# Optimization experiments

Measured on AMD Instinct MI355X. Metric: run time of the kernel, lower is better.

The kernel has to match this reference:

```python
import jax, jax.numpy as jnp
import numpy as np

DIM, HEADS, RANK = 768, 12, 64
HEAD_DIM = DIM // HEADS

def _xavier(key, shape):
    fan_in, fan_out = shape[1], shape[0]
    std = (2.0 / (fan_in + fan_out)) ** 0.5
    return std * jax.random.normal(key, shape, dtype=jnp.float32)

def setup_inputs() -> dict:
    key = jax.random.key(0)
    ks = jax.random.split(key, 12)
    B, N = 8, 1024
    x = jax.random.normal(ks[0], (B, N, DIM), dtype=jnp.float32)
    params = {}
    for i, nm in enumerate(['Q', 'K', 'V']):
        params[f'W_{nm}0'] = _xavier(ks[1 + 3 * i], (DIM, RANK))
        params[f'W_{nm}1'] = _xavier(ks[2 + 3 * i], (HEADS, RANK))
        params[f'W_{nm}2'] = _xavier(ks[3 + 3 * i], (HEAD_DIM, RANK))
    proj_w = _xavier(ks[10], (DIM, DIM))
    proj_b = jnp.zeros((DIM,), dtype=jnp.float32)
    return dict(x=x, W_Q0=params['W_Q0'], W_Q1=params['W_Q1'], W_Q2=params['W_Q2'],
                W_K0=params['W_K0'], W_K1=params['W_K1'], W_K2=params['W_K2'],
                W_V0=params['W_V0'], W_V1=params['W_V1'], W_V2=params['W_V2'],
                proj_w=proj_w, proj_b=proj_b)

def _cp_proj(xh, W2, W1, W0, B, N, H, hd):
    # xh: [B,N,H,hd]; contract head_dim with W2 and heads with W1 -> [B,N,R], then expand to dim via W0
    t = jnp.einsum('blnd,dr,nr->blr', xh, W2, W1)
    out = jnp.einsum('blr,mr->blm', t, W0)          # [B,N,dim]
    return out.reshape(B, N, H, hd).transpose(0, 2, 1, 3)  # [B,H,N,hd]

def reference(x, W_Q0, W_Q1, W_Q2, W_K0, W_K1, W_K2, W_V0, W_V1, W_V2, proj_w, proj_b):
    B, N, C = x.shape
    H = W_Q1.shape[0]
    hd = C // H
    scale = hd ** -0.5
    xh = x.reshape(B, N, H, hd)
    q = _cp_proj(xh, W_Q2, W_Q1, W_Q0, B, N, H, hd)
    k = _cp_proj(xh, W_K2, W_K1, W_K0, B, N, H, hd)
    v = _cp_proj(xh, W_V2, W_V1, W_V0, B, N, H, hd)
    attn = jax.nn.softmax(jnp.einsum('bhqd,bhkd->bhqk', q, k) * scale, axis=-1)
    out = jnp.einsum('bhqk,bhkd->bhqd', attn, v).transpose(0, 2, 1, 3).reshape(B, N, C)
    return out @ proj_w.T + proj_b
```

## Files before the change

### kernel.cpp

```cpp
#include <hip/hip_runtime.h>

typedef unsigned short u16;
typedef __attribute__((ext_vector_type(8))) short bf16x8;
typedef __attribute__((ext_vector_type(4))) float f32x4;
typedef __attribute__((ext_vector_type(4))) unsigned short u16x4;
typedef __attribute__((ext_vector_type(8))) unsigned short u16x8;

#define AS1 __attribute__((address_space(1)))
#define AS3 __attribute__((address_space(3)))

__device__ __forceinline__ float b2f(u16 s) {
    return __uint_as_float(((unsigned)s) << 16);
}
__device__ __forceinline__ u16 f2b(float f) {
    unsigned u = __float_as_uint(f);
    unsigned r = 0x7fffu + ((u >> 16) & 1u);
    return (u16)((u + r) >> 16);
}

__device__ __forceinline__ unsigned packtrunc(float p0, float p1) {
#if __has_builtin(__builtin_amdgcn_perm)
    return __builtin_amdgcn_perm(__float_as_uint(p1), __float_as_uint(p0), 0x07060302u);
#else
    return (__float_as_uint(p0) >> 16) | (__float_as_uint(p1) & 0xffff0000u);
#endif
}

__device__ __forceinline__ void g2l16(const u16* g, u16* l) {
    __builtin_amdgcn_global_load_lds((const AS1 void*)g, (AS3 void*)l, 16, 0, 0);
}

#if __has_builtin(__builtin_amdgcn_exp2f)
#define EXP2(x) __builtin_amdgcn_exp2f(x)
#else
#define EXP2(x) exp2f(x)
#endif

__global__ __launch_bounds__(256) void build_prep(
    const float* __restrict__ Wq0, const float* __restrict__ Wq1, const float* __restrict__ Wq2,
    const float* __restrict__ Wk0, const float* __restrict__ Wk1, const float* __restrict__ Wk2,
    const float* __restrict__ Wv0, const float* __restrict__ Wv1, const float* __restrict__ Wv2,
    const float* __restrict__ PW,
    u16* __restrict__ G, u16* __restrict__ MqkT, u16* __restrict__ Dcat)
{
    const int bx = blockIdx.x;
    const int t = threadIdx.x;
    if (bx < 576) {
        const int idx = bx * 256 + t;
        const int row = idx / 768, c = idx - row * 768;
        const int which = row >> 6, r = row & 63;
        const int h = c >> 6, d = c & 63;
        const float* W1 = (which == 0) ? Wq1 : (which == 1) ? Wk1 : Wv1;
        const float* W2 = (which == 0) ? Wq2 : (which == 1) ? Wk2 : Wv2;
        G[idx] = f2b(W1[h * 64 + r] * W2[d * 64 + r]);
    } else if (bx < 624) {
        __shared__ float wq[64 * 65];
        __shared__ float wk[64 * 65];
        const int hq = bx - 576;
        const int h = hq >> 2, quarter = hq & 3;
        const float qs = 0.125f * 1.4426950408889634f;
        for (int i = t; i < 4096; i += 256) {
            const int dd = i >> 6, r = i & 63;
            wq[dd * 65 + r] = Wq0[(h * 64 + dd) * 64 + r] * qs;
            wk[dd * 65 + r] = Wk0[(h * 64 + dd) * 64 + r];
        }
        __syncthreads();
        const int j0 = quarter * 1024 + t * 4;
        const int r2 = j0 >> 6, r1b = j0 & 63;
        u16x4 pk;
#pragma unroll
        for (int jj = 0; jj < 4; ++jj) {
            float acc = 0.f;
#pragma unroll
            for (int dd = 0; dd < 64; ++dd)
                acc += wk[dd * 65 + r2] * wq[dd * 65 + r1b + jj];
            ((u16*)&pk)[jj] = f2b(acc);
        }
        *(u16x4*)(MqkT + (size_t)(h * 64 + r2) * 64 + r1b) = pk;
    } else {
        __shared__ float w0s[64 * 65];
        __shared__ float pws[32 * 65];
        const int hb = bx - 624;
        const int h = hb / 24, mBase = (hb - h * 24) * 32;
        for (int i = t; i < 4096; i += 256) {
            const int d = i >> 6, r = i & 63;
            w0s[d * 65 + r] = Wv0[(h * 64 + d) * 64 + r];
        }
        for (int i = t; i < 2048; i += 256) {
            const int mi = i >> 6, d = i & 63;
            pws[mi * 65 + d] = PW[(size_t)(mBase + mi) * 768 + h * 64 + d];
        }
        __syncthreads();
        const int r = t & 63, mi0 = t >> 6;
        float w0c[64];
#pragma unroll
        for (int d = 0; d < 64; ++d) w0c[d] = w0s[d * 65 + r];
        for (int mi = mi0; mi < 32; mi += 4) {
            float acc = 0.f;
#pragma unroll
            for (int d = 0; d < 64; ++d) acc += pws[mi * 65 + d] * w0c[d];
            Dcat[(size_t)(mBase + mi) * 768 + h * 64 + r] = f2b(acc);
        }
    }
}

__global__ __launch_bounds__(256, 2) void gemm_t(
    const float* __restrict__ X, const u16* __restrict__ G,
    u16* __restrict__ T, u16* __restrict__ tvt)
{
    __shared__ u16 As[64 * 32];
    __shared__ u16 Bs[64 * 32];

    const int tid = threadIdx.x;
    const int lane = tid & 63, wv = tid >> 6;
    const int l15 = lane & 15, quad = lane >> 4;

    const int lin = blockIdx.x + 3 * blockIdx.y;
    const int xcd = lin & 7, j = lin >> 3;
    const int col = j % 3, rowhi = j / 3;
    const int rowBase = (rowhi * 8 + xcd) * 64;
    const int colBase = col * 64;

    const int srow = tid >> 2;
    const int scol = (tid & 3) * 8;
    const float* aS = X + (size_t)(rowBase + srow) * 768 + scol;
    const u16*  bS  = G + (size_t)(colBase + srow) * 768 + scol;

    float4 a0 = *(const float4*)(aS);
    float4 a1 = *(const float4*)(aS + 4);
    int4   b0 = *(const int4*)(bS);

    const f32x4 zero4 = {0.f, 0.f, 0.f, 0.f};
    f32x4 acc[4];
#pragma unroll
    for (int tn = 0; tn < 4; ++tn) acc[tn] = zero4;

    for (int kk = 0; kk < 768; kk += 32) {
        __syncthreads();
        u16x8 ap;
        ap[0] = f2b(a0.x); ap[1] = f2b(a0.y); ap[2] = f2b(a0.z); ap[3] = f2b(a0.w);
        ap[4] = f2b(a1.x); ap[5] = f2b(a1.y); ap[6] = f2b(a1.z); ap[7] = f2b(a1.w);
        *(u16x8*)&As[srow * 32 + scol] = ap;
        *(int4*)&Bs[srow * 32 + scol]  = b0;
        __syncthreads();

        if (kk < 736) {
            a0 = *(const float4*)(aS + kk + 32);
            a1 = *(const float4*)(aS + kk + 36);
            b0 = *(const int4*)(bS + kk + 32);
        }

        const bf16x8 af = *(const bf16x8*)(As + (wv * 16 + l15) * 32 + quad * 8);
#pragma unroll
        for (int tn = 0; tn < 4; ++tn) {
            const bf16x8 bf = *(const bf16x8*)(Bs + (tn * 16 + l15) * 32 + quad * 8);
            acc[tn] = __builtin_amdgcn_mfma_f32_16x16x32_bf16(af, bf, acc[tn], 0, 0, 0);
        }
    }

    if (colBase < 128) {
#pragma unroll
        for (int tn = 0; tn < 4; ++tn) {
            const int c = colBase + tn * 16 + l15;
#pragma unroll
            for (int r = 0; r < 4; ++r) {
                const int grow = rowBase + wv * 16 + quad * 4 + r;
                T[(size_t)grow * 128 + c] = f2b(acc[tn][r]);
            }
        }
    } else {
#pragma unroll
        for (int tn = 0; tn < 4; ++tn) {
            const int rr = tn * 16 + l15;
            const int grow = rowBase + wv * 16 + quad * 4;
            u16x4 pk;
            pk.x = f2b(acc[tn][0]); pk.y = f2b(acc[tn][1]);
            pk.z = f2b(acc[tn][2]); pk.w = f2b(acc[tn][3]);
            *(u16x4*)(tvt + (size_t)rr * 8192 + grow) = pk;
        }
    }
}

__global__ __launch_bounds__(256, 3) void flash_attn8(
    const u16* __restrict__ T, const u16* __restrict__ MqkT,
    const u16* __restrict__ tvt, u16* __restrict__ Z)
{
    const int bh = blockIdx.x;
    const int qt = blockIdx.y;
    const int b = bh / 12, h = bh - b * 12;
    const u16* qp = T + ((size_t)b * 1024 + qt * 128) * 128;
    const u16* kp = T + (size_t)b * 1024 * 128 + 64;
    const u16* vp = tvt + b * 1024;

    __shared__ u16 Ks[64][72];
    __shared__ u16 Vs[64][72];
    __shared__ u16 Ws[128][72];

    const int t = threadIdx.x;
    const int lane = t & 63, wv = t >> 6;
    const int l15 = lane & 15, quad = lane >> 4;

    bf16x8 qf[2][2];
#pragma unroll
    for (int qg = 0; qg < 2; ++qg) {
        const u16* qrow = qp + (size_t)(wv * 32 + qg * 16 + l15) * 128;
        qf[qg][0] = *(const bf16x8*)(qrow + quad * 8);
        qf[qg][1] = *(const bf16x8*)(qrow + 32 + quad * 8);
    }

    const int srow = t >> 2;
    const int scol = (t & 3) * 16;
    const int p5 = srow & 31;
    const int lrow = (srow & 32) | ((p5 & 4) << 2) | ((p5 & 16) >> 1)
                   | ((p5 & 8) >> 1) | (p5 & 3);

    bf16x8 vone = {};
    if (l15 == 0) {
#pragma unroll
        for (int j = 0; j < 8; ++j) vone[j] = (short)0x3F80;
    }

    int4 kr0 = *(const int4*)(kp + (size_t)srow * 128 + scol);
    int4 kr1 = *(const int4*)(kp + (size_t)srow * 128 + scol + 8);
    int4 vr0 = *(const int4*)(vp + (size_t)srow * 8192 + scol);
    int4 vr1 = *(const int4*)(vp + (size_t)srow * 8192 + scol + 8);

    const f32x4 zero4 = {0.f, 0.f, 0.f, 0.f};
    {
        f32x4 Wt[2][4];
#pragma unroll
        for (int qg = 0; qg < 2; ++qg)
#pragma unroll
            for (int tn = 0; tn < 4; ++tn) Wt[qg][tn] = zero4;
#pragma unroll
        for (int ks = 0; ks < 2; ++ks) {
#pragma unroll
            for (int tn = 0; tn < 4; ++tn) {
                const bf16x8 mb = *(const bf16x8*)(
                    MqkT + (size_t)(h * 64 + tn * 16 + l15) * 64 + ks * 32 + quad * 8);
                Wt[0][tn] = __builtin_amdgcn_mfma_f32_16x16x32_bf16(qf[0][ks], mb, Wt[0][tn], 0, 0, 0);
                Wt[1][tn] = __builtin_amdgcn_mfma_f32_16x16x32_bf16(qf[1][ks], mb, Wt[1][tn], 0, 0, 0);
            }
        }
#pragma unroll
        for (int qg = 0; qg < 2; ++qg)
#pragma unroll
            for (int tn = 0; tn < 4; ++tn)
#pragma unroll
                for (int r = 0; r < 4; ++r)
                    Ws[wv * 32 + qg * 16 + quad * 4 + r][tn * 16 + l15] = f2b(Wt[qg][tn][r]);
    }
    __syncthreads();
    bf16x8 wf[2][2];
#pragma unroll
    for (int qg = 0; qg < 2; ++qg) {
        wf[qg][0] = *(const bf16x8*)&Ws[wv * 32 + qg * 16 + l15][quad * 8];
        wf[qg][1] = *(const bf16x8*)&Ws[wv * 32 + qg * 16 + l15][32 + quad * 8];
    }

    f32x4 o_acc[2][4];
    f32x4 Lacc[2] = {zero4, zero4};
#pragma unroll
    for (int qg = 0; qg < 2; ++qg)
#pragma unroll
        for (int tn = 0; tn < 4; ++tn) o_acc[qg][tn] = zero4;

    for (int kt = 0; kt < 16; ++kt) {
        __syncthreads();
        *(int4*)&Ks[lrow][scol]     = kr0;
        *(int4*)&Ks[lrow][scol + 8] = kr1;
        *(int4*)&Vs[srow][scol]     = vr0;
        *(int4*)&Vs[srow][scol + 8] = vr1;
        __syncthreads();

        if (kt < 15) {
            kr0 = *(const int4*)(kp + (size_t)((kt + 1) * 64 + srow) * 128 + scol);
            kr1 = *(const int4*)(kp + (size_t)((kt + 1) * 64 + srow) * 128 + scol + 8);
            vr0 = *(const int4*)(vp + (size_t)srow * 8192 + (kt + 1) * 64 + scol);
            vr1 = *(const int4*)(vp + (size_t)srow * 8192 + (kt + 1) * 64 + scol + 8);
        }

        f32x4 Sacc[2][4];
#pragma unroll
        for (int qg = 0; qg < 2; ++qg)
#pragma unroll
            for (int tk = 0; tk < 4; ++tk) Sacc[qg][tk] = zero4;
#pragma unroll
        for (int ks = 0; ks < 2; ++ks) {
#pragma unroll
            for (int tk = 0; tk < 4; ++tk) {
                const bf16x8 kf = *(const bf16x8*)&Ks[tk * 16 + l15][ks * 32 + quad * 8];
                Sacc[0][tk] = __builtin_amdgcn_mfma_f32_16x16x32_bf16(kf, wf[0][ks], Sacc[0][tk], 0, 0, 0);
                Sacc[1][tk] = __builtin_amdgcn_mfma_f32_16x16x32_bf16(kf, wf[1][ks], Sacc[1][tk], 0, 0, 0);
            }
        }

        union { bf16x8 v; unsigned u[4]; } pf[2][2];
#pragma unroll
        for (int qg = 0; qg < 2; ++qg)
#pragma unroll
            for (int tk = 0; tk < 4; ++tk) {
                const float p0 = EXP2(Sacc[qg][tk][0]);
                const float p1 = EXP2(Sacc[qg][tk][1]);
                const float p2 = EXP2(Sacc[qg][tk][2]);
                const float p3 = EXP2(Sacc[qg][tk][3]);
                const int g = tk >> 1, hf = (tk & 1) * 2;
                pf[qg][g].u[hf + 0] = packtrunc(p0, p1);
                pf[qg][g].u[hf + 1] = packtrunc(p2, p3);
            }

#pragma unroll
        for (int g = 0; g < 2; ++g) {
#pragma unroll
            for (int tn = 0; tn < 4; ++tn) {
                const bf16x8 vf = *(const bf16x8*)&Vs[tn * 16 + l15][g * 32 + quad * 8];
                o_acc[0][tn] = __builtin_amdgcn_mfma_f32_16x16x32_bf16(pf[0][g].v, vf, o_acc[0][tn], 0, 0, 0);
                o_acc[1][tn] = __builtin_amdgcn_mfma_f32_16x16x32_bf16(pf[1][g].v, vf, o_acc[1][tn], 0, 0, 0);
            }
            Lacc[0] = __builtin_amdgcn_mfma_f32_16x16x32_bf16(pf[0][g].v, vone, Lacc[0], 0, 0, 0);
            Lacc[1] = __builtin_amdgcn_mfma_f32_16x16x32_bf16(pf[1][g].v, vone, Lacc[1], 0, 0, 0);
        }
    }

#pragma unroll
    for (int qg = 0; qg < 2; ++qg) {
#pragma unroll
        for (int r = 0; r < 4; ++r) {
            const float Lv = __shfl(Lacc[qg][r], quad << 4, 64);
            const float inv = 1.0f / Lv;
            const int token = qt * 128 + wv * 32 + qg * 16 + quad * 4 + r;
#pragma unroll
            for (int tn = 0; tn < 4; ++tn) {
                const int col = h * 64 + tn * 16 + l15;
                Z[(size_t)(b * 1024 + token) * 768 + col] = f2b(o_acc[qg][tn][r] * inv);
            }
        }
    }
}

__global__ __launch_bounds__(256, 3) void gemm_out(
    const u16* __restrict__ A, const u16* __restrict__ Bt,
    float* __restrict__ C, const float* __restrict__ bias)
{
    __shared__ u16 As[128 * 32];
    __shared__ u16 Bs[64 * 32];

    const int tid  = threadIdx.x;
    const int lane = tid & 63, wv = tid >> 6;
    const int l15  = lane & 15, quad = lane >> 4;

    const int lin = blockIdx.x + 12 * blockIdx.y;
    const int xcd = lin & 7, j = lin >> 3;
    const int colT = j % 12, rowhi = j / 12;
    const int rowBase = (rowhi * 8 + xcd) * 128;
    const int colBase = colT * 64;

    const int srowA = wv * 32 + (lane >> 2);
    const int srowB = wv * 16 + (lane >> 2);
    const int scol  = (lane & 3) * 8;
    const u16* aSrc = A  + (size_t)(rowBase + srowA) * 768 + scol;
    const u16* bSrc = Bt + (size_t)(colBase + srowB) * 768 + scol;
    u16* aDst = As + wv * 1024;
    u16* bDst = Bs + wv * 512;

    const f32x4 zero4 = {0.f, 0.f, 0.f, 0.f};
    f32x4 acc[2][4];
#pragma unroll
    for (int tm = 0; tm < 2; ++tm)
#pragma unroll
        for (int tn = 0; tn < 4; ++tn) acc[tm][tn] = zero4;

    for (int kk = 0; kk < 768; kk += 32) {
        __syncthreads();
        g2l16(aSrc + kk,            aDst);
        g2l16(aSrc + kk + 16 * 768, aDst + 512);
        g2l16(bSrc + kk,            bDst);
        __syncthreads();

        bf16x8 af[2], bfm[4];
#pragma unroll
        for (int t = 0; t < 2; ++t)
            af[t]  = *(const bf16x8*)(As + (wv * 32 + t * 16 + l15) * 32 + quad * 8);
#pragma unroll
        for (int t = 0; t < 4; ++t)
            bfm[t] = *(const bf16x8*)(Bs + (t * 16 + l15) * 32 + quad * 8);
#pragma unroll
        for (int tm = 0; tm < 2; ++tm)
#pragma unroll
            for (int tn = 0; tn < 4; ++tn)
                acc[tm][tn] = __builtin_amdgcn_mfma_f32_16x16x32_bf16(
                    af[tm], bfm[tn], acc[tm][tn], 0, 0, 0);
    }

#pragma unroll
    for (int tm = 0; tm < 2; ++tm) {
        const int grow = rowBase + wv * 32 + tm * 16 + quad * 4;
#pragma unroll
        for (int tn = 0; tn < 4; ++tn) {
            const int gcol = colBase + tn * 16 + l15;
            const float bv = bias[gcol];
#pragma unroll
            for (int r = 0; r < 4; ++r)
                C[(size_t)(grow + r) * 768 + gcol] = acc[tm][tn][r] + bv;
        }
    }
}

extern "C" void kernel_launch(void* const* d_in, const int* in_sizes, int n_in,
                              void* d_out, int out_size, void* d_ws, size_t ws_size,
                              hipStream_t stream)
{
    const float* x      = (const float*)d_in[0];
    const float* Wq0    = (const float*)d_in[1];
    const float* Wq1    = (const float*)d_in[2];
    const float* Wq2    = (const float*)d_in[3];
    const float* Wk0    = (const float*)d_in[4];
    const float* Wk1    = (const float*)d_in[5];
    const float* Wk2    = (const float*)d_in[6];
    const float* Wv0    = (const float*)d_in[7];
    const float* Wv1    = (const float*)d_in[8];
    const float* Wv2    = (const float*)d_in[9];
    const float* proj_w = (const float*)d_in[10];
    const float* proj_b = (const float*)d_in[11];
    float* outp = (float*)d_out;

    char* ws = (char*)d_ws;
    u16* T    = (u16*)ws;
    u16* tvt  = (u16*)(ws + 2097152);
    u16* G    = (u16*)(ws + 3145728);
    u16* MqkT = (u16*)(ws + 3440640);
    u16* Dcat = (u16*)(ws + 3538944);
    u16* Zcat = (u16*)(ws + 4718592);

    build_prep<<<912, 256, 0, stream>>>(Wq0, Wq1, Wq2, Wk0, Wk1, Wk2, Wv0, Wv1, Wv2,
                                        proj_w, G, MqkT, Dcat);
    gemm_t<<<dim3(3, 128), 256, 0, stream>>>(x, G, T, tvt);
    flash_attn8<<<dim3(96, 8), 256, 0, stream>>>(T, MqkT, tvt, Zcat);
    gemm_out<<<dim3(12, 64), 256, 0, stream>>>(Zcat, Dcat, outp, proj_b);
}
```

Baseline: 170.5 us.

## Double-buffer K/V tiles in LDS and compute softmax row sums with VALU

The attention kernel now keeps two LDS buffers for K/V tiles. It stages the next tile's register-prefetched data into the alternate buffer while computing on the current one, so each iteration needs one barrier instead of two. The row-sum MFMA against a ones vector is replaced by per-lane VALU accumulation of the truncated probabilities, followed by cross-lane shuffles, and s_setprio hints wrap the MFMA sections. This trades extra LDS footprint and VALU adds for fewer MFMAs and less barrier stalling.

```diff
diff --git a/kernel.cpp b/kernel.cpp
--- a/kernel.cpp
+++ b/kernel.cpp
@@ -24,6 +24,10 @@
 #else
     return (__float_as_uint(p0) >> 16) | (__float_as_uint(p1) & 0xffff0000u);
 #endif
+}
+
+__device__ __forceinline__ float truncbf(float p) {
+    return __uint_as_float(__float_as_uint(p) & 0xffff0000u);
 }
 
 __device__ __forceinline__ void g2l16(const u16* g, u16* l) {
@@ -181,7 +185,7 @@
     }
 }
 
-__global__ __launch_bounds__(256, 3) void flash_attn8(
+__global__ __launch_bounds__(256, 3) void flash_attn9(
     const u16* __restrict__ T, const u16* __restrict__ MqkT,
     const u16* __restrict__ tvt, u16* __restrict__ Z)
 {
@@ -192,9 +196,8 @@
     const u16* kp = T + (size_t)b * 1024 * 128 + 64;
     const u16* vp = tvt + b * 1024;
 
-    __shared__ u16 Ks[64][72];
-    __shared__ u16 Vs[64][72];
-    __shared__ u16 Ws[128][72];
+    __shared__ u16 B0raw[2 * 64 * 72];
+    __shared__ u16 B1raw[2 * 64 * 72];
 
     const int t = threadIdx.x;
     const int lane = t & 63, wv = t >> 6;
@@ -214,12 +217,6 @@
     const int lrow = (srow & 32) | ((p5 & 4) << 2) | ((p5 & 16) >> 1)
                    | ((p5 & 8) >> 1) | (p5 & 3);
 
-    bf16x8 vone = {};
-    if (l15 == 0) {
-#pragma unroll
-        for (int j = 0; j < 8; ++j) vone[j] = (short)0x3F80;
-    }
-
     int4 kr0 = *(const int4*)(kp + (size_t)srow * 128 + scol);
     int4 kr1 = *(const int4*)(kp + (size_t)srow * 128 + scol + 8);
     int4 vr0 = *(const int4*)(vp + (size_t)srow * 8192 + scol);
@@ -248,36 +245,49 @@
             for (int tn = 0; tn < 4; ++tn)
 #pragma unroll
                 for (int r = 0; r < 4; ++r)
-                    Ws[wv * 32 + qg * 16 + quad * 4 + r][tn * 16 + l15] = f2b(Wt[qg][tn][r]);
+                    B1raw[(wv * 32 + qg * 16 + quad * 4 + r) * 72 + tn * 16 + l15] =
+                        f2b(Wt[qg][tn][r]);
     }
     __syncthreads();
     bf16x8 wf[2][2];
 #pragma unroll
     for (int qg = 0; qg < 2; ++qg) {
-        wf[qg][0] = *(const bf16x8*)&Ws[wv * 32 + qg * 16 + l15][quad * 8];
-        wf[qg][1] = *(const bf16x8*)&Ws[wv * 32 + qg * 16 + l15][32 + quad * 8];
-    }
+        wf[qg][0] = *(const bf16x8*)&B1raw[(wv * 32 + qg * 16 + l15) * 72 + quad * 8];
+        wf[qg][1] = *(const bf16x8*)&B1raw[(wv * 32 + qg * 16 + l15) * 72 + 32 + quad * 8];
+    }
+
+    *(int4*)&B0raw[lrow * 72 + scol]                 = kr0;
+    *(int4*)&B0raw[lrow * 72 + scol + 8]             = kr1;
+    *(int4*)&B0raw[64 * 72 + srow * 72 + scol]       = vr0;
+    *(int4*)&B0raw[64 * 72 + srow * 72 + scol + 8]   = vr1;
+    kr0 = *(const int4*)(kp + (size_t)(64 + srow) * 128 + scol);
+    kr1 = *(const int4*)(kp + (size_t)(64 + srow) * 128 + scol + 8);
+    vr0 = *(const int4*)(vp + (size_t)srow * 8192 + 64 + scol);
+    vr1 = *(const int4*)(vp + (size_t)srow * 8192 + 64 + scol + 8);
+    __syncthreads();
 
     f32x4 o_acc[2][4];
-    f32x4 Lacc[2] = {zero4, zero4};
+    float Lsum[2] = {0.f, 0.f};
 #pragma unroll
     for (int qg = 0; qg < 2; ++qg)
 #pragma unroll
         for (int tn = 0; tn < 4; ++tn) o_acc[qg][tn] = zero4;
 
     for (int kt = 0; kt < 16; ++kt) {
-        __syncthreads();
-        *(int4*)&Ks[lrow][scol]     = kr0;
-        *(int4*)&Ks[lrow][scol + 8] = kr1;
-        *(int4*)&Vs[srow][scol]     = vr0;
-        *(int4*)&Vs[srow][scol + 8] = vr1;
-        __syncthreads();
-
+        u16* const kb = (kt & 1) ? B1raw : B0raw;
+        u16* const vb = kb + 64 * 72;
         if (kt < 15) {
-            kr0 = *(const int4*)(kp + (size_t)((kt + 1) * 64 + srow) * 128 + scol);
-            kr1 = *(const int4*)(kp + (size_t)((kt + 1) * 64 + srow) * 128 + scol + 8);
-            vr0 = *(const int4*)(vp + (size_t)srow * 8192 + (kt + 1) * 64 + scol);
-            vr1 = *(const int4*)(vp + (size_t)srow * 8192 + (kt + 1) * 64 + scol + 8);
+            u16* const kn = (kt & 1) ? B0raw : B1raw;
+            *(int4*)&kn[lrow * 72 + scol]               = kr0;
+            *(int4*)&kn[lrow * 72 + scol + 8]           = kr1;
+            *(int4*)&kn[64 * 72 + srow * 72 + scol]     = vr0;
+            *(int4*)&kn[64 * 72 + srow * 72 + scol + 8] = vr1;
+            if (kt < 14) {
+                kr0 = *(const int4*)(kp + (size_t)((kt + 2) * 64 + srow) * 128 + scol);
+                kr1 = *(const int4*)(kp + (size_t)((kt + 2) * 64 + srow) * 128 + scol + 8);
+                vr0 = *(const int4*)(vp + (size_t)srow * 8192 + (kt + 2) * 64 + scol);
+                vr1 = *(const int4*)(vp + (size_t)srow * 8192 + (kt + 2) * 64 + scol + 8);
+            }
         }
 
         f32x4 Sacc[2][4];
@@ -285,15 +295,17 @@
         for (int qg = 0; qg < 2; ++qg)
 #pragma unroll
             for (int tk = 0; tk < 4; ++tk) Sacc[qg][tk] = zero4;
+        __builtin_amdgcn_s_setprio(1);
 #pragma unroll
         for (int ks = 0; ks < 2; ++ks) {
 #pragma unroll
             for (int tk = 0; tk < 4; ++tk) {
-                const bf16x8 kf = *(const bf16x8*)&Ks[tk * 16 + l15][ks * 32 + quad * 8];
+                const bf16x8 kf = *(const bf16x8*)&kb[(tk * 16 + l15) * 72 + ks * 32 + quad * 8];
                 Sacc[0][tk] = __builtin_amdgcn_mfma_f32_16x16x32_bf16(kf, wf[0][ks], Sacc[0][tk], 0, 0, 0);
                 Sacc[1][tk] = __builtin_amdgcn_mfma_f32_16x16x32_bf16(kf, wf[1][ks], Sacc[1][tk], 0, 0, 0);
             }
         }
+        __builtin_amdgcn_s_setprio(0);
 
         union { bf16x8 v; unsigned u[4]; } pf[2][2];
 #pragma unroll
@@ -307,26 +319,32 @@
                 const int g = tk >> 1, hf = (tk & 1) * 2;
                 pf[qg][g].u[hf + 0] = packtrunc(p0, p1);
                 pf[qg][g].u[hf + 1] = packtrunc(p2, p3);
-            }
-
+                Lsum[qg] += (truncbf(p0) + truncbf(p1)) + (truncbf(p2) + truncbf(p3));
+            }
+
+        __builtin_amdgcn_s_setprio(1);
 #pragma unroll
         for (int g = 0; g < 2; ++g) {
 #pragma unroll
             for (int tn = 0; tn < 4; ++tn) {
-                const bf16x8 vf = *(const bf16x8*)&Vs[tn * 16 + l15][g * 32 + quad * 8];
+                const bf16x8 vf = *(const bf16x8*)&vb[(tn * 16 + l15) * 72 + g * 32 + quad * 8];
                 o_acc[0][tn] = __builtin_amdgcn_mfma_f32_16x16x32_bf16(pf[0][g].v, vf, o_acc[0][tn], 0, 0, 0);
                 o_acc[1][tn] = __builtin_amdgcn_mfma_f32_16x16x32_bf16(pf[1][g].v, vf, o_acc[1][tn], 0, 0, 0);
             }
-            Lacc[0] = __builtin_amdgcn_mfma_f32_16x16x32_bf16(pf[0][g].v, vone, Lacc[0], 0, 0, 0);
-            Lacc[1] = __builtin_amdgcn_mfma_f32_16x16x32_bf16(pf[1][g].v, vone, Lacc[1], 0, 0, 0);
-        }
+        }
+        __builtin_amdgcn_s_setprio(0);
+
+        __syncthreads();
     }
 
 #pragma unroll
     for (int qg = 0; qg < 2; ++qg) {
+        float Ls = Lsum[qg];
+        Ls += __shfl_xor(Ls, 16, 64);
+        Ls += __shfl_xor(Ls, 32, 64);
 #pragma unroll
         for (int r = 0; r < 4; ++r) {
-            const float Lv = __shfl(Lacc[qg][r], quad << 4, 64);
+            const float Lv = __shfl(Ls, quad * 4 + r, 64);
             const float inv = 1.0f / Lv;
             const int token = qt * 128 + wv * 32 + qg * 16 + quad * 4 + r;
 #pragma unroll
@@ -435,6 +453,6 @@
     build_prep<<<912, 256, 0, stream>>>(Wq0, Wq1, Wq2, Wk0, Wk1, Wk2, Wv0, Wv1, Wv2,
                                         proj_w, G, MqkT, Dcat);
     gemm_t<<<dim3(3, 128), 256, 0, stream>>>(x, G, T, tvt);
-    flash_attn8<<<dim3(96, 8), 256, 0, stream>>>(T, MqkT, tvt, Zcat);
+    flash_attn9<<<dim3(96, 8), 256, 0, stream>>>(T, MqkT, tvt, Zcat);
     gemm_out<<<dim3(12, 64), 256, 0, stream>>>(Zcat, Dcat, outp, proj_b);
 }
```

Measured after the change: 178.0 us. 4.4% more time.
